# Kernel optimization log

Measured on AMD Instinct MI355X. Metric: run time of the kernel, lower is better.

Reference implementation:

```python
import jax, jax.numpy as jnp
import numpy as np

ALPHA_SCALE = 8.0  # exp(alpha_log_scale) where alpha_log_scale = log(8)
EPS = 1e-6


def _depthwise_causal_conv(x, conv_w, conv_b):
    # x: [N, H, T], conv_w: [H, 1, K], conv_b: [H]
    K = conv_w.shape[-1]
    y = jax.lax.conv_general_dilated(
        x, conv_w,
        window_strides=(1,),
        padding=[(K - 1, 0)],  # causal: torch pads both sides then slices [..., :T]
        dimension_numbers=("NCH", "OIH", "NCH"),
        feature_group_count=x.shape[1],
    )
    return y + conv_b[None, :, None]


def _linear_scan(alpha, x):
    # h_t = alpha_t * h_{t-1} + x_t along time axis=1; alpha, x: [N, T, H]
    def combine(c1, c2):
        a1, b1 = c1
        a2, b2 = c2
        return a1 * a2, a2 * b1 + b2
    _, h = jax.lax.associative_scan(combine, (alpha, x), axis=1)
    return h


def setup_inputs() -> dict:
    key = jax.random.key(0)
    ks = jax.random.split(key, 8)
    N, T, D = 4, 4096, 1024
    H, K = 1536, 4
    return {
        "x": jax.random.normal(ks[0], (N, T, D), dtype=jnp.float32),
        "W_in": jax.random.normal(ks[1], (2 * H, D), dtype=jnp.float32) * (D ** -0.5),
        "conv_w": jax.random.normal(ks[2], (H, 1, K), dtype=jnp.float32) * 0.1,
        "conv_b": jax.random.normal(ks[3], (H,), dtype=jnp.float32) * 0.1,
        "W_g": jax.random.normal(ks[4], (2 * H, H), dtype=jnp.float32) * (H ** -0.5),
        "b_g": jax.random.normal(ks[5], (2 * H,), dtype=jnp.float32) * 0.1,
        "forget_base": jax.random.normal(ks[6], (H,), dtype=jnp.float32),
        "W_out": jax.random.normal(ks[7], (D, H), dtype=jnp.float32) * (H ** -0.5),
    }


def reference(x, W_in, conv_w, conv_b, W_g, b_g, forget_base, W_out):
    H = W_g.shape[1]
    # input projection and split into gate / x branch
    gx = jnp.einsum("ntd,hd->nth", x, W_in)  # [N,T,2H]
    gate, xb = gx[..., :H], gx[..., H:]
    # depthwise causal conv
    xb = _depthwise_causal_conv(jnp.swapaxes(xb, 1, 2), conv_w, conv_b)
    xb = jnp.swapaxes(xb, 1, 2)  # [N,T,H]
    # gates
    fg = jnp.einsum("nth,gh->ntg", xb, W_g) + b_g  # [N,T,2H]
    forget, inp = fg[..., :H], fg[..., H:]
    # RG-LRU gating
    alpha = jnp.exp(-ALPHA_SCALE * jax.nn.softplus(forget_base) * jax.nn.sigmoid(forget))
    beta = jnp.sqrt(1.0 - alpha ** 2 + EPS)
    xs = beta * jax.nn.sigmoid(inp) * xb
    # linear recurrence h_t = alpha_t * h_{t-1} + xs_t
    h = _linear_scan(alpha, xs)
    # output projection with GeLU-gated hidden state (torch gelu = exact erf form)
    return jnp.einsum("nth,dh->ntd", jax.nn.gelu(gate, approximate=False) * h, W_out)
```

## Files before the change

kernel.cpp:

```cpp
#include <hip/hip_runtime.h>
#include <stdint.h>
#include <math.h>

#define N_B 4
#define T_S 4096
#define D_M 1024
#define H_M 1536
#define NT  (N_B * T_S)
#define G2  (2 * H_M)
#define LCH 64
#define NCH 64

typedef __attribute__((ext_vector_type(8))) short short8;
typedef __attribute__((ext_vector_type(4))) float floatx4;

__device__ __forceinline__ unsigned short f2bf(float f) {
  unsigned u = __float_as_uint(f);
  u += 0x7fff + ((u >> 16) & 1);
  return (unsigned short)(u >> 16);
}
__device__ __forceinline__ float bf2f(unsigned short u) {
  return __uint_as_float(((unsigned)u) << 16);
}
__device__ __forceinline__ float bf_lo(unsigned p) { return __uint_as_float(p << 16); }
__device__ __forceinline__ float bf_hi(unsigned p) { return __uint_as_float(p & 0xffff0000u); }
__device__ __forceinline__ unsigned bf_pack(float lo, float hi) {
  return ((unsigned)f2bf(lo)) | (((unsigned)f2bf(hi)) << 16);
}
__device__ __forceinline__ float sigmoidf_(float x) { return 1.f / (1.f + __expf(-x)); }
__device__ __forceinline__ float softplusf_(float x) {
  return (x > 20.f) ? x : log1pf(__expf(x));
}
__device__ __forceinline__ float geluf_(float x) {
  return 0.5f * x * (1.f + erff(x * 0.70710678118654752f));
}

__global__ void zero_out(float* __restrict__ out, int n) {
  int i = blockIdx.x * 256 + threadIdx.x;
  if (i < n) out[i] = 0.f;
}

#define N4_X   (NT * D_M / 4)
#define N4_WIN (G2 * D_M / 4)
#define N4_WG  (G2 * H_M / 4)
__global__ void cvt3_bf16(const float* __restrict__ x, unsigned short* __restrict__ x16,
                          const float* __restrict__ win, unsigned short* __restrict__ win16,
                          const float* __restrict__ wg, unsigned short* __restrict__ wg16) {
  int i = blockIdx.x * 256 + threadIdx.x;
  const float* in; unsigned short* out;
  if (i < N4_X)                { in = x;   out = x16; }
  else if (i < N4_X + N4_WIN)  { in = win; out = win16; i -= N4_X; }
  else if (i < N4_X + N4_WIN + N4_WG) { in = wg; out = wg16; i -= N4_X + N4_WIN; }
  else return;
  float4 v = ((const float4*)in)[i];
  ushort4 o;
  o.x = f2bf(v.x); o.y = f2bf(v.y); o.z = f2bf(v.z); o.w = f2bf(v.w);
  ((ushort4*)out)[i] = o;
}

__global__ void cvt_bf16(const float* __restrict__ in, unsigned short* __restrict__ out, int n4) {
  int i = blockIdx.x * 256 + threadIdx.x;
  if (i >= n4) return;
  float4 v = ((const float4*)in)[i];
  ushort4 o;
  o.x = f2bf(v.x); o.y = f2bf(v.y); o.z = f2bf(v.z); o.w = f2bf(v.w);
  ((ushort4*)out)[i] = o;
}

#define TM 256
#define TN 256

__device__ __forceinline__ void stage16(const unsigned short* g, unsigned short* l) {
  __builtin_amdgcn_global_load_lds((__attribute__((address_space(1))) void*)g,
                                   (__attribute__((address_space(3))) void*)l, 16, 0, 0);
}

template<bool BIAS, bool OUT_BF16, bool SPLIT>
__global__ __launch_bounds__(512, 2)
void gemm_bt8(const unsigned short* __restrict__ A,
              const unsigned short* __restrict__ B,
              void* __restrict__ Cv, void* __restrict__ Cv2,
              const float* __restrict__ bias,
              int N, int K) {
  __shared__ __align__(16) unsigned short As[2][2][8192];
  __shared__ __align__(16) unsigned short Bs[2][2][8192];
  const int tid  = threadIdx.x;
  const int lane = tid & 63;
  const int wave = tid >> 6;
  const int wr = wave >> 2;
  const int wc = wave & 3;

  const int gx  = gridDim.x;
  const int nwg = gx * gridDim.y;
  const int bid = blockIdx.y * gx + blockIdx.x;
  const int cpx = nwg >> 3;
  const int swz = (bid & 7) * cpx + (bid >> 3);
  const int bm = (swz / gx) * TM;
  const int bn = (swz % gx) * TN;

  floatx4 acc[8][4];
#pragma unroll
  for (int i = 0; i < 8; i++)
#pragma unroll
    for (int j = 0; j < 4; j++)
      acc[i][j] = (floatx4){0.f, 0.f, 0.f, 0.f};

  const int r0_ = tid >> 3;
  const int g8  = ((tid & 7) ^ (r0_ & 7)) * 8;
  const unsigned short* Ag[2][2];
  const unsigned short* Bg[2][2];
#pragma unroll
  for (int h = 0; h < 2; ++h)
#pragma unroll
    for (int u = 0; u < 2; ++u) {
      Ag[h][u] = A + (size_t)(bm + h * 128 + r0_ + 64 * u) * K + g8;
      Bg[h][u] = B + (size_t)(bn + h * 128 + r0_ + 64 * u) * K + g8;
    }
  const int ldd = tid * 8;

#define STAGE_A(bu, h, kb) do { \
    stage16(Ag[h][0] + (kb), &As[bu][h][ldd]); \
    stage16(Ag[h][1] + (kb), &As[bu][h][ldd + 4096]); } while (0)
#define STAGE_B(bu, h, kb) do { \
    stage16(Bg[h][0] + (kb), &Bs[bu][h][ldd]); \
    stage16(Bg[h][1] + (kb), &Bs[bu][h][ldd + 4096]); } while (0)

  const int fr = lane & 15;
  const int kq = lane >> 4;
  const int e8 = fr & 7;
  const int px0 = (kq ^ e8) * 8;
  const int px1 = ((4 + kq) ^ e8) * 8;
  const int arow = fr * 64;
  const int brow = ((wc & 1) * 64 + fr) * 64;

  const int nt = K >> 6;
  short8 af[2][2], bfr[4][2];

  STAGE_A(0, 0, 0); STAGE_A(0, 1, 0);
  STAGE_B(0, 0, 0); STAGE_B(0, 1, 0);
  if (nt > 1) { STAGE_B(1, 0, 64); STAGE_B(1, 1, 64); }

  for (int t = 0; t < nt; ++t) {
    const int par = t & 1;
    const int kn1 = (t + 1) << 6;
    const int kn2 = (t + 2) << 6;
    const bool s1 = (t + 1 < nt);
    const bool s2 = (t + 2 < nt);

    if (s1) { asm volatile("s_waitcnt vmcnt(4)" ::: "memory"); }
    else    { asm volatile("s_waitcnt vmcnt(0)" ::: "memory"); }
    __builtin_amdgcn_s_barrier();

    const unsigned short* Ab = &As[par][wr][0];
    const unsigned short* Bb = &Bs[par][wc >> 1][0];

#pragma unroll
    for (int j = 0; j < 4; ++j) {
      bfr[j][0] = *(const short8*)(Bb + brow + j * 1024 + px0);
      bfr[j][1] = *(const short8*)(Bb + brow + j * 1024 + px1);
    }
#pragma unroll
    for (int ii = 0; ii < 2; ++ii) {
      af[ii][0] = *(const short8*)(Ab + arow + ii * 1024 + px0);
      af[ii][1] = *(const short8*)(Ab + arow + ii * 1024 + px1);
    }
    if (s1) STAGE_A(par ^ 1, 0, kn1);
    __builtin_amdgcn_s_setprio(1);
#pragma unroll
    for (int kh = 0; kh < 2; ++kh)
#pragma unroll
      for (int ii = 0; ii < 2; ++ii)
#pragma unroll
        for (int j = 0; j < 4; ++j)
          acc[ii][j] = __builtin_amdgcn_mfma_f32_16x16x32_bf16(af[ii][kh], bfr[j][kh], acc[ii][j], 0, 0, 0);
    __builtin_amdgcn_s_setprio(0);
    __builtin_amdgcn_s_barrier();

#pragma unroll
    for (int ii = 0; ii < 2; ++ii) {
      af[ii][0] = *(const short8*)(Ab + arow + (2048 + ii * 1024) + px0);
      af[ii][1] = *(const short8*)(Ab + arow + (2048 + ii * 1024) + px1);
    }
    if (s1) STAGE_A(par ^ 1, 1, kn1);
    if (s2) STAGE_B(par, 0, kn2);
    __builtin_amdgcn_s_setprio(1);
#pragma unroll
    for (int kh = 0; kh < 2; ++kh)
#pragma unroll
      for (int ii = 0; ii < 2; ++ii)
#pragma unroll
        for (int j = 0; j < 4; ++j)
          acc[2 + ii][j] = __builtin_amdgcn_mfma_f32_16x16x32_bf16(af[ii][kh], bfr[j][kh], acc[2 + ii][j], 0, 0, 0);
    __builtin_amdgcn_s_setprio(0);

#pragma unroll
    for (int ii = 0; ii < 2; ++ii) {
      af[ii][0] = *(const short8*)(Ab + arow + (4096 + ii * 1024) + px0);
      af[ii][1] = *(const short8*)(Ab + arow + (4096 + ii * 1024) + px1);
    }
    if (s2) STAGE_B(par, 1, kn2);
    __builtin_amdgcn_s_setprio(1);
#pragma unroll
    for (int kh = 0; kh < 2; ++kh)
#pragma unroll
      for (int ii = 0; ii < 2; ++ii)
#pragma unroll
        for (int j = 0; j < 4; ++j)
          acc[4 + ii][j] = __builtin_amdgcn_mfma_f32_16x16x32_bf16(af[ii][kh], bfr[j][kh], acc[4 + ii][j], 0, 0, 0);
    __builtin_amdgcn_s_setprio(0);

#pragma unroll
    for (int ii = 0; ii < 2; ++ii) {
      af[ii][0] = *(const short8*)(Ab + arow + (6144 + ii * 1024) + px0);
      af[ii][1] = *(const short8*)(Ab + arow + (6144 + ii * 1024) + px1);
    }
    __builtin_amdgcn_s_setprio(1);
#pragma unroll
    for (int kh = 0; kh < 2; ++kh)
#pragma unroll
      for (int ii = 0; ii < 2; ++ii)
#pragma unroll
        for (int j = 0; j < 4; ++j)
          acc[6 + ii][j] = __builtin_amdgcn_mfma_f32_16x16x32_bf16(af[ii][kh], bfr[j][kh], acc[6 + ii][j], 0, 0, 0);
    __builtin_amdgcn_s_setprio(0);
  }
#undef STAGE_A
#undef STAGE_B

  const int half  = SPLIT ? (N >> 1) : N;
  const bool hi   = SPLIT && (bn >= half);
  void* Cb        = hi ? Cv2 : Cv;
  const int coff  = hi ? half : 0;
  const int cn = lane & 15;
  const int rb = (lane >> 4) * 4;
  float bv[4];
#pragma unroll
  for (int j = 0; j < 4; ++j)
    bv[j] = BIAS ? bias[bn + wc * 64 + j * 16 + cn] : 0.f;
  const int col0 = bn + wc * 64 + cn - coff;
#pragma unroll
  for (int i = 0; i < 8; ++i) {
    const int row0 = bm + wr * 128 + i * 16 + rb;
#pragma unroll
    for (int r = 0; r < 4; ++r) {
      const size_t rowb = (size_t)(row0 + r) * half + col0;
#pragma unroll
      for (int j = 0; j < 4; ++j) {
        float v = acc[i][j][r] + bv[j];
        if (OUT_BF16) ((unsigned short*)Cb)[rowb + j * 16] = f2bf(v);
        else          ((float*)Cb)[rowb + j * 16] = v;
      }
    }
  }
}

__global__ void conv_dw(const unsigned int* __restrict__ xbpre2, const float* __restrict__ cw,
                        const float* __restrict__ cb, unsigned int* __restrict__ xbc2) {
  int i0 = blockIdx.x * 256 + threadIdx.x;
  int t = blockIdx.y;
  size_t nt = (size_t)blockIdx.z * T_S + t;
  const int h = 2 * i0;
  const float4 wa = ((const float4*)cw)[h];
  const float4 wb = ((const float4*)cw)[h + 1];
  const float2 cb2 = ((const float2*)cb)[i0];
  size_t base = nt * (H_M / 2) + i0;
  unsigned p0 = xbpre2[base];
  float aa = cb2.x + wa.w * bf_lo(p0);
  float ab = cb2.y + wb.w * bf_hi(p0);
  if (t >= 1) { unsigned p = xbpre2[base - H_M / 2];
    aa += wa.z * bf_lo(p); ab += wb.z * bf_hi(p); }
  if (t >= 2) { unsigned p = xbpre2[base - 2 * (size_t)(H_M / 2)];
    aa += wa.y * bf_lo(p); ab += wb.y * bf_hi(p); }
  if (t >= 3) { unsigned p = xbpre2[base - 3 * (size_t)(H_M / 2)];
    aa += wa.x * bf_lo(p); ab += wb.x * bf_hi(p); }
  xbc2[base] = bf_pack(aa, ab);
}

__global__ void scan_A(const unsigned int* __restrict__ fg2, const unsigned int* __restrict__ xbc2,
                       const float* __restrict__ fb,
                       float2* __restrict__ cA2, float2* __restrict__ cS2) {
  int i0 = blockIdx.x * 256 + threadIdx.x;
  int ch = blockIdx.y;
  int n = blockIdx.z;
  const float2 fb2 = ((const float2*)fb)[i0];
  const float c8a = 8.f * softplusf_(fb2.x);
  const float c8b = 8.f * softplusf_(fb2.y);
  float apa = 1.f, sa = 0.f, apb = 1.f, sb = 0.f;
  size_t r = (size_t)n * T_S + (size_t)ch * LCH;
  for (int i = 0; i < LCH; i++, r++) {
    unsigned pf = fg2[r * (G2 / 2) + i0];
    unsigned pi = fg2[r * (G2 / 2) + H_M / 2 + i0];
    unsigned px = xbc2[r * (H_M / 2) + i0];
    float alpha_a = __expf(-c8a * sigmoidf_(bf_lo(pf)));
    float alpha_b = __expf(-c8b * sigmoidf_(bf_hi(pf)));
    float beta_a = sqrtf(1.f - alpha_a * alpha_a + 1e-6f);
    float beta_b = sqrtf(1.f - alpha_b * alpha_b + 1e-6f);
    sa = alpha_a * sa + beta_a * sigmoidf_(bf_lo(pi)) * bf_lo(px);
    sb = alpha_b * sb + beta_b * sigmoidf_(bf_hi(pi)) * bf_hi(px);
    apa *= alpha_a;
    apb *= alpha_b;
  }
  size_t o = ((size_t)n * NCH + ch) * (H_M / 2) + i0;
  cA2[o] = make_float2(apa, apb);
  cS2[o] = make_float2(sa, sb);
}

__global__ void scan_C(const unsigned int* __restrict__ fg2, const unsigned int* __restrict__ xbc2,
                       const float* __restrict__ fb,
                       const float2* __restrict__ cA2, const float2* __restrict__ cS2,
                       unsigned int* gateh2) {
  int i0 = blockIdx.x * 256 + threadIdx.x;
  int ch = blockIdx.y;
  int n = blockIdx.z;
  const float2 fb2 = ((const float2*)fb)[i0];
  const float c8a = 8.f * softplusf_(fb2.x);
  const float c8b = 8.f * softplusf_(fb2.y);
  float sa = 0.f, sb = 0.f;
  for (int c = 0; c < ch; c++) {
    size_t o = ((size_t)n * NCH + c) * (H_M / 2) + i0;
    float2 a = cA2[o], s = cS2[o];
    sa = a.x * sa + s.x;
    sb = a.y * sb + s.y;
  }
  size_t r = (size_t)n * T_S + (size_t)ch * LCH;
  for (int i = 0; i < LCH; i++, r++) {
    unsigned pf = fg2[r * (G2 / 2) + i0];
    unsigned pi = fg2[r * (G2 / 2) + H_M / 2 + i0];
    unsigned px = xbc2[r * (H_M / 2) + i0];
    float alpha_a = __expf(-c8a * sigmoidf_(bf_lo(pf)));
    float alpha_b = __expf(-c8b * sigmoidf_(bf_hi(pf)));
    float beta_a = sqrtf(1.f - alpha_a * alpha_a + 1e-6f);
    float beta_b = sqrtf(1.f - alpha_b * alpha_b + 1e-6f);
    sa = alpha_a * sa + beta_a * sigmoidf_(bf_lo(pi)) * bf_lo(px);
    sb = alpha_b * sb + beta_b * sigmoidf_(bf_hi(pi)) * bf_hi(px);
    unsigned pg = gateh2[r * (H_M / 2) + i0];
    gateh2[r * (H_M / 2) + i0] = bf_pack(geluf_(bf_lo(pg)) * sa, geluf_(bf_hi(pg)) * sb);
  }
}

extern "C" void kernel_launch(void* const* d_in, const int* in_sizes, int n_in,
                              void* d_out, int out_size, void* d_ws, size_t ws_size,
                              hipStream_t stream) {
  const float* x    = (const float*)d_in[0];
  const float* Win  = (const float*)d_in[1];
  const float* cw   = (const float*)d_in[2];
  const float* cb   = (const float*)d_in[3];
  const float* Wg   = (const float*)d_in[4];
  const float* bg   = (const float*)d_in[5];
  const float* fb   = (const float*)d_in[6];
  const float* Wout = (const float*)d_in[7];
  float* out = (float*)d_out;
  (void)in_sizes; (void)n_in;

  const size_t S = (size_t)NT * H_M * 2;
  const size_t needed = 4 * S + (size_t)G2 * H_M * 2;
  if (ws_size < needed) {
    zero_out<<<(out_size + 255) / 256, 256, 0, stream>>>(out, out_size);
    return;
  }

  char* base = (char*)d_ws;
  unsigned short* gate16  = (unsigned short*)(base);
  unsigned short* xbpre16 = (unsigned short*)(base + S);
  unsigned short* fg16    = (unsigned short*)(base + S);
  unsigned short* x16     = (unsigned short*)(base + 2 * S);
  unsigned short* Win16   = (unsigned short*)(base + 2 * S + (size_t)NT * D_M * 2);
  unsigned short* xbc16   = (unsigned short*)(base + 3 * S);
  unsigned short* Wg16    = (unsigned short*)(base + 4 * S);
  float* cA    = (float*)(base + 4 * S);
  float* cS    = cA + (size_t)N_B * NCH * H_M;
  unsigned short* Wout16  = (unsigned short*)(cS + (size_t)N_B * NCH * H_M);

  cvt3_bf16<<<(N4_X + N4_WIN + N4_WG + 255) / 256, 256, 0, stream>>>(
      x, x16, Win, Win16, Wg, Wg16);

  gemm_bt8<false, true, true><<<dim3(G2 / TN, NT / TM), 512, 0, stream>>>(
      x16, Win16, gate16, xbpre16, nullptr, G2, D_M);
  conv_dw<<<dim3(H_M / 512, T_S, N_B), 256, 0, stream>>>(
      (const unsigned int*)xbpre16, cw, cb, (unsigned int*)xbc16);
  gemm_bt8<true, true, false><<<dim3(G2 / TN, NT / TM), 512, 0, stream>>>(
      xbc16, Wg16, fg16, nullptr, bg, G2, H_M);
  cvt_bf16<<<(D_M * H_M / 4 + 255) / 256, 256, 0, stream>>>(Wout, Wout16, D_M * H_M / 4);
  scan_A<<<dim3(H_M / 512, NCH, N_B), 256, 0, stream>>>(
      (const unsigned int*)fg16, (const unsigned int*)xbc16, fb, (float2*)cA, (float2*)cS);
  scan_C<<<dim3(H_M / 512, NCH, N_B), 256, 0, stream>>>(
      (const unsigned int*)fg16, (const unsigned int*)xbc16, fb,
      (const float2*)cA, (const float2*)cS, (unsigned int*)gate16);
  gemm_bt8<false, false, false><<<dim3(D_M / TN, NT / TM), 512, 0, stream>>>(
      gate16, Wout16, out, nullptr, nullptr, D_M, H_M);
}
```

Before: 655.7 us.

## Load GEMM A fragments directly from global into registers, bypassing LDS

Removes the LDS staging buffer for the A operand. Each wave now loads its A fragments straight from global memory into registers, software-pipelined one quarter ahead. B stays staged in LDS, but its prefetch depth drops from two tiles to one, and each iteration waits on vmcnt(0). This halves LDS use and cuts LDS traffic and barriers, at the cost of uncoalesced, redundant global reads of A (four waves share the same rows) and less latency hiding for B.

```diff
diff --git a/kernel.cpp b/kernel.cpp
--- a/kernel.cpp
+++ b/kernel.cpp
@@ -82,7 +82,6 @@
               void* __restrict__ Cv, void* __restrict__ Cv2,
               const float* __restrict__ bias,
               int N, int K) {
-  __shared__ __align__(16) unsigned short As[2][2][8192];
   __shared__ __align__(16) unsigned short Bs[2][2][8192];
   const int tid  = threadIdx.x;
   const int lane = tid & 63;
@@ -107,20 +106,14 @@
 
   const int r0_ = tid >> 3;
   const int g8  = ((tid & 7) ^ (r0_ & 7)) * 8;
-  const unsigned short* Ag[2][2];
   const unsigned short* Bg[2][2];
 #pragma unroll
   for (int h = 0; h < 2; ++h)
 #pragma unroll
-    for (int u = 0; u < 2; ++u) {
-      Ag[h][u] = A + (size_t)(bm + h * 128 + r0_ + 64 * u) * K + g8;
+    for (int u = 0; u < 2; ++u)
       Bg[h][u] = B + (size_t)(bn + h * 128 + r0_ + 64 * u) * K + g8;
-    }
   const int ldd = tid * 8;
 
-#define STAGE_A(bu, h, kb) do { \
-    stage16(Ag[h][0] + (kb), &As[bu][h][ldd]); \
-    stage16(Ag[h][1] + (kb), &As[bu][h][ldd + 4096]); } while (0)
 #define STAGE_B(bu, h, kb) do { \
     stage16(Bg[h][0] + (kb), &Bs[bu][h][ldd]); \
     stage16(Bg[h][1] + (kb), &Bs[bu][h][ldd + 4096]); } while (0)
@@ -130,28 +123,45 @@
   const int e8 = fr & 7;
   const int px0 = (kq ^ e8) * 8;
   const int px1 = ((4 + kq) ^ e8) * 8;
-  const int arow = fr * 64;
   const int brow = ((wc & 1) * 64 + fr) * 64;
+  const unsigned short* gA = A + (size_t)(bm + wr * 128 + fr) * K + kq * 8;
+
+#define LOAD_AF(dst, mq, kb) do { \
+    _Pragma("unroll") \
+    for (int ii = 0; ii < 2; ++ii) { \
+      const unsigned short* ap = gA + (size_t)((mq) * 32 + ii * 16) * K + (kb); \
+      dst[ii][0] = *(const short8*)(ap); \
+      dst[ii][1] = *(const short8*)(ap + 32); \
+    } } while (0)
+
+#define MFMA_Q(base, set) do { \
+    __builtin_amdgcn_s_setprio(1); \
+    _Pragma("unroll") \
+    for (int kh = 0; kh < 2; ++kh) \
+      _Pragma("unroll") \
+      for (int ii = 0; ii < 2; ++ii) \
+        _Pragma("unroll") \
+        for (int j = 0; j < 4; ++j) \
+          acc[(base) + ii][j] = __builtin_amdgcn_mfma_f32_16x16x32_bf16( \
+              set[ii][kh], bfr[j][kh], acc[(base) + ii][j], 0, 0, 0); \
+    __builtin_amdgcn_s_setprio(0); } while (0)
 
   const int nt = K >> 6;
-  short8 af[2][2], bfr[4][2];
-
-  STAGE_A(0, 0, 0); STAGE_A(0, 1, 0);
+  short8 af0[2][2], af1[2][2], af2[2][2], af3[2][2], bfr[4][2];
+
   STAGE_B(0, 0, 0); STAGE_B(0, 1, 0);
-  if (nt > 1) { STAGE_B(1, 0, 64); STAGE_B(1, 1, 64); }
+  LOAD_AF(af0, 0, 0);
 
   for (int t = 0; t < nt; ++t) {
     const int par = t & 1;
-    const int kn1 = (t + 1) << 6;
-    const int kn2 = (t + 2) << 6;
+    const int dn  = par ^ 1;
+    const int k0  = t << 6;
+    const int kn1 = k0 + 64;
     const bool s1 = (t + 1 < nt);
-    const bool s2 = (t + 2 < nt);
-
-    if (s1) { asm volatile("s_waitcnt vmcnt(4)" ::: "memory"); }
-    else    { asm volatile("s_waitcnt vmcnt(0)" ::: "memory"); }
+
+    asm volatile("s_waitcnt vmcnt(0)" ::: "memory");
     __builtin_amdgcn_s_barrier();
 
-    const unsigned short* Ab = &As[par][wr][0];
     const unsigned short* Bb = &Bs[par][wc >> 1][0];
 
 #pragma unroll
@@ -159,73 +169,23 @@
       bfr[j][0] = *(const short8*)(Bb + brow + j * 1024 + px0);
       bfr[j][1] = *(const short8*)(Bb + brow + j * 1024 + px1);
     }
-#pragma unroll
-    for (int ii = 0; ii < 2; ++ii) {
-      af[ii][0] = *(const short8*)(Ab + arow + ii * 1024 + px0);
-      af[ii][1] = *(const short8*)(Ab + arow + ii * 1024 + px1);
-    }
-    if (s1) STAGE_A(par ^ 1, 0, kn1);
-    __builtin_amdgcn_s_setprio(1);
-#pragma unroll
-    for (int kh = 0; kh < 2; ++kh)
-#pragma unroll
-      for (int ii = 0; ii < 2; ++ii)
-#pragma unroll
-        for (int j = 0; j < 4; ++j)
-          acc[ii][j] = __builtin_amdgcn_mfma_f32_16x16x32_bf16(af[ii][kh], bfr[j][kh], acc[ii][j], 0, 0, 0);
-    __builtin_amdgcn_s_setprio(0);
-    __builtin_amdgcn_s_barrier();
-
-#pragma unroll
-    for (int ii = 0; ii < 2; ++ii) {
-      af[ii][0] = *(const short8*)(Ab + arow + (2048 + ii * 1024) + px0);
-      af[ii][1] = *(const short8*)(Ab + arow + (2048 + ii * 1024) + px1);
-    }
-    if (s1) STAGE_A(par ^ 1, 1, kn1);
-    if (s2) STAGE_B(par, 0, kn2);
-    __builtin_amdgcn_s_setprio(1);
-#pragma unroll
-    for (int kh = 0; kh < 2; ++kh)
-#pragma unroll
-      for (int ii = 0; ii < 2; ++ii)
-#pragma unroll
-        for (int j = 0; j < 4; ++j)
-          acc[2 + ii][j] = __builtin_amdgcn_mfma_f32_16x16x32_bf16(af[ii][kh], bfr[j][kh], acc[2 + ii][j], 0, 0, 0);
-    __builtin_amdgcn_s_setprio(0);
-
-#pragma unroll
-    for (int ii = 0; ii < 2; ++ii) {
-      af[ii][0] = *(const short8*)(Ab + arow + (4096 + ii * 1024) + px0);
-      af[ii][1] = *(const short8*)(Ab + arow + (4096 + ii * 1024) + px1);
-    }
-    if (s2) STAGE_B(par, 1, kn2);
-    __builtin_amdgcn_s_setprio(1);
-#pragma unroll
-    for (int kh = 0; kh < 2; ++kh)
-#pragma unroll
-      for (int ii = 0; ii < 2; ++ii)
-#pragma unroll
-        for (int j = 0; j < 4; ++j)
-          acc[4 + ii][j] = __builtin_amdgcn_mfma_f32_16x16x32_bf16(af[ii][kh], bfr[j][kh], acc[4 + ii][j], 0, 0, 0);
-    __builtin_amdgcn_s_setprio(0);
-
-#pragma unroll
-    for (int ii = 0; ii < 2; ++ii) {
-      af[ii][0] = *(const short8*)(Ab + arow + (6144 + ii * 1024) + px0);
-      af[ii][1] = *(const short8*)(Ab + arow + (6144 + ii * 1024) + px1);
-    }
-    __builtin_amdgcn_s_setprio(1);
-#pragma unroll
-    for (int kh = 0; kh < 2; ++kh)
-#pragma unroll
-      for (int ii = 0; ii < 2; ++ii)
-#pragma unroll
-        for (int j = 0; j < 4; ++j)
-          acc[6 + ii][j] = __builtin_amdgcn_mfma_f32_16x16x32_bf16(af[ii][kh], bfr[j][kh], acc[6 + ii][j], 0, 0, 0);
-    __builtin_amdgcn_s_setprio(0);
-  }
-#undef STAGE_A
+    LOAD_AF(af1, 1, k0);
+    if (s1) STAGE_B(dn, 0, kn1);
+    MFMA_Q(0, af0);
+
+    LOAD_AF(af2, 2, k0);
+    if (s1) STAGE_B(dn, 1, kn1);
+    MFMA_Q(2, af1);
+
+    LOAD_AF(af3, 3, k0);
+    MFMA_Q(4, af2);
+
+    if (s1) LOAD_AF(af0, 0, kn1);
+    MFMA_Q(6, af3);
+  }
 #undef STAGE_B
+#undef LOAD_AF
+#undef MFMA_Q
 
   const int half  = SPLIT ? (N >> 1) : N;
   const bool hi   = SPLIT && (bn >= half);
```

Measured after the change: 1.005 ms. +53.3%, slower.
